# Optimization experiments

Hardware: AMD Instinct MI355X
Metric: run time of the kernel (lower is better)

The kernel has to match this reference:

```python
import jax, jax.numpy as jnp
import numpy as np

EMBED = 1024
HEADS = 16
HEAD_DIM = EMBED // HEADS
LN_EPS = 1e-5
XNORM_GAMMA = 0.01


def xnorm(x, gamma):
    # x * gamma / ||x||_4 along last dim (keepdim)
    norm4 = jnp.sum(x ** 4, axis=-1, keepdims=True) ** 0.25
    return x * gamma / norm4


def setup_inputs() -> dict:
    key = jax.random.key(0)
    ks = jax.random.split(key, 12)
    B, S = 2, 2048
    sc_hd = 1.0 / np.sqrt(HEAD_DIM)
    sc_e = 1.0 / np.sqrt(EMBED)
    return {
        "value": jax.random.normal(ks[0], (B, S, EMBED), jnp.float32),
        "key": jax.random.normal(ks[1], (B, S, EMBED), jnp.float32),
        "query": jax.random.normal(ks[2], (B, S, EMBED), jnp.float32),
        # per-head projections, torch Linear convention: y = x @ W.T
        "Wq": jax.random.normal(ks[3], (HEAD_DIM, HEAD_DIM), jnp.float32) * sc_hd,
        "Wk": jax.random.normal(ks[4], (HEAD_DIM, HEAD_DIM), jnp.float32) * sc_hd,
        "Wv": jax.random.normal(ks[5], (HEAD_DIM, HEAD_DIM), jnp.float32) * sc_hd,
        "Wo": jax.random.normal(ks[6], (EMBED, EMBED), jnp.float32) * sc_e,
        "bo": jnp.zeros((EMBED,), jnp.float32),
        "ln_w": jnp.ones((EMBED,), jnp.float32),
        "ln_b": jnp.zeros((EMBED,), jnp.float32),
        "Wsq": jax.random.normal(ks[7], (EMBED, EMBED), jnp.float32) * sc_e,
        "bsq": jnp.zeros((EMBED,), jnp.float32),
    }


def reference(value, key, query, Wq, Wk, Wv, Wo, bo, ln_w, ln_b, Wsq, bsq):
    B, S, E = query.shape
    # split heads: [B, S, H, D]
    v = value.reshape(B, S, HEADS, HEAD_DIM)
    k = key.reshape(B, S, HEADS, HEAD_DIM)
    q = query.reshape(B, S, HEADS, HEAD_DIM)
    v = jnp.einsum('nshd,ed->nshe', v, Wv)
    k = jnp.einsum('nshd,ed->nshe', k, Wk)
    q = jnp.einsum('nshd,ed->nshe', q, Wq)
    # energy: [B, H, Sq, Sk]
    energy = jnp.einsum('nqhd,nkhd->nhqk', q, k)
    energy_n = xnorm(energy, XNORM_GAMMA)
    v_n = xnorm(v, XNORM_GAMMA)
    out = jnp.einsum('nhql,nlhd->nqhd', energy_n, v_n).reshape(B, S, E)
    attn = out @ Wo.T + bo
    # LayerNorm(attention + query) over embed dim
    x = attn + query
    mu = jnp.mean(x, axis=-1, keepdims=True)
    var = jnp.mean((x - mu) ** 2, axis=-1, keepdims=True)
    x = (x - mu) / jnp.sqrt(var + LN_EPS) * ln_w + ln_b
    # SE gating: x * sigmoid(Linear(x))
    gate = jax.nn.sigmoid(x @ Wsq.T + bsq)
    return x * gate
```

## Files before the change

### kernel.cpp

```cpp
#include <hip/hip_runtime.h>
#include <stdint.h>

#define B_ 2
#define S_ 2048
#define E_ 1024
#define H_ 16
#define HD_ 64
#define N_ (B_*S_)
#define BH_ (B_*H_)
#define GAMMA 0.01f

typedef __attribute__((ext_vector_type(8))) short bf16x8;
typedef __attribute__((ext_vector_type(4))) float f32x4;
typedef __attribute__((ext_vector_type(2))) float f32x2;
typedef __attribute__((ext_vector_type(16))) float f32x16;
typedef unsigned short u16;
typedef unsigned int u32;

#define SWZ(row, kb) ((kb) ^ (((row)&7)<<4))

__device__ __forceinline__ u16 f2bf(float f){
  union { float f; u32 u; } v; v.f = f;
  return (u16)((v.u + 0x7FFFu + ((v.u>>16)&1u)) >> 16);
}

__device__ __forceinline__ float bf2f(u16 u){
  union { u32 u; float f; } v; v.u = ((u32)u)<<16; return v.f;
}

__device__ __forceinline__ u32 cvt_pk_bf16(float lo, float hi){
  u32 r; asm("v_cvt_pk_bf16_f32 %0, %1, %2" : "=v"(r) : "v"(lo), "v"(hi)); return r;
}

__device__ __forceinline__ uint4 pack8(float4 a, float4 b){
  uint4 r;
  r.x = cvt_pk_bf16(a.x, a.y);
  r.y = cvt_pk_bf16(a.z, a.w);
  r.z = cvt_pk_bf16(b.x, b.y);
  r.w = cvt_pk_bf16(b.z, b.w);
  return r;
}

__device__ __forceinline__ bf16x8 ldfrag(const unsigned char* base, int row, int kbyte){
  return *reinterpret_cast<const bf16x8*>(base + row*128 + SWZ(row, kbyte));
}

__device__ __forceinline__ void gl_lds16(const void* g, void* l){
  __builtin_amdgcn_global_load_lds(
      (const __attribute__((address_space(1))) unsigned int*)g,
      (__attribute__((address_space(3))) unsigned int*)l, 16, 0, 0);
}

__device__ __forceinline__ void proj_mfma(const unsigned char* X, const unsigned char* W,
                                          int wid, int l15, int g4, f32x4 acc[4])
{
  f32x4 z = {0.f,0.f,0.f,0.f};
  acc[0]=z; acc[1]=z; acc[2]=z; acc[3]=z;
  #pragma unroll
  for (int kk=0;kk<2;++kk){
    int kbyte = kk*64 + g4*16;
    bf16x8 a = ldfrag(X, wid*16 + l15, kbyte);
    #pragma unroll
    for (int t=0;t<4;++t){
      bf16x8 w = ldfrag(W, t*16 + l15, kbyte);
      acc[t] = __builtin_amdgcn_mfma_f32_16x16x32_bf16(a, w, acc[t], 0, 0, 0);
    }
  }
}

__global__ __launch_bounds__(256) void k_proj(
    const float* __restrict__ qin, const float* __restrict__ kin, const float* __restrict__ vin,
    const float* __restrict__ Wq, const float* __restrict__ Wk, const float* __restrict__ Wv,
    u16* __restrict__ qp, u16* __restrict__ kp, u16* __restrict__ kpT, u16* __restrict__ vnT,
    const float* __restrict__ Wo, const float* __restrict__ Wsq,
    u16* __restrict__ wo16, u16* __restrict__ wsq16)
{
  __shared__ alignas(16) unsigned char sm[49152];
  if (blockIdx.y >= H_){
    int cblk = (blockIdx.y - H_)*64 + blockIdx.x;
    int n4 = (E_*E_)/4;
    for (int i = cblk*256 + threadIdx.x; i < 2*n4; i += 128*256){
      const float4* src; ushort4* dst; int j;
      if (i < n4){ src=(const float4*)Wo;  dst=(ushort4*)wo16;  j=i; }
      else       { src=(const float4*)Wsq; dst=(ushort4*)wsq16; j=i-n4; }
      float4 v = src[j];
      ushort4 p; p.x=f2bf(v.x); p.y=f2bf(v.y); p.z=f2bf(v.z); p.w=f2bf(v.w);
      dst[j] = p;
    }
    return;
  }
  const int XQ=0, XK=8192, XV=16384, WQS=24576, WKS=32768, WVS=40960;
  int tid = threadIdx.x, lane = tid&63, wid = tid>>6;
  int l15 = lane&15, g4 = lane>>4;
  int tb = blockIdx.x*64;
  int h  = blockIdx.y;
  int b  = tb >> 11;
  int sbase = tb & 2047;
  int bh = b*H_ + h;

  {
    int rl = tid>>2;
    int d0 = (tid&3)*16;
    const float* xs[3] = { qin, kin, vin };
    const float* wsrc[3] = { Wq, Wk, Wv };
    const int xoff[3] = {XQ,XK,XV}, woff[3] = {WQS,WKS,WVS};
    #pragma unroll
    for (int m3=0;m3<3;++m3){
      const float4* gx = reinterpret_cast<const float4*>(xs[m3] + (size_t)(tb+rl)*E_ + h*HD_ + d0);
      float4 a=gx[0], bb=gx[1], c=gx[2], d=gx[3];
      *(uint4*)(sm + xoff[m3] + rl*128 + SWZ(rl, d0*2))    = pack8(a,bb);
      *(uint4*)(sm + xoff[m3] + rl*128 + SWZ(rl, d0*2+16)) = pack8(c,d);
      const float4* gw = reinterpret_cast<const float4*>(wsrc[m3] + rl*64 + d0);
      float4 e=gw[0], f=gw[1], g2=gw[2], h2=gw[3];
      *(uint4*)(sm + woff[m3] + rl*128 + SWZ(rl, d0*2))    = pack8(e,f);
      *(uint4*)(sm + woff[m3] + rl*128 + SWZ(rl, d0*2+16)) = pack8(g2,h2);
    }
  }
  __syncthreads();

  f32x4 qacc[4], kacc[4], vacc[4];
  proj_mfma(sm+XQ, sm+WQS, wid, l15, g4, qacc);
  proj_mfma(sm+XK, sm+WKS, wid, l15, g4, kacc);
  proj_mfma(sm+XV, sm+WVS, wid, l15, g4, vacc);

  {
    float p4r[4] = {0.f,0.f,0.f,0.f};
    #pragma unroll
    for (int t=0;t<4;++t)
      #pragma unroll
      for (int r=0;r<4;++r){ float e = vacc[t][r]; float e2 = e*e; p4r[r] += e2*e2; }
    #pragma unroll
    for (int r=0;r<4;++r){
      float p = p4r[r];
      p += __shfl_xor(p,1); p += __shfl_xor(p,2); p += __shfl_xor(p,4); p += __shfl_xor(p,8);
      p4r[r] = GAMMA / sqrtf(sqrtf(p));
    }
    #pragma unroll
    for (int t=0;t<4;++t)
      #pragma unroll
      for (int r=0;r<4;++r) vacc[t][r] *= p4r[r];
  }

  __syncthreads();

  #pragma unroll
  for (int t=0;t<4;++t){
    int dd = t*16 + l15;
    #pragma unroll
    for (int r=0;r<4;++r){
      int tokl = wid*16 + g4*4 + r;
      *(u16*)(sm + XQ + tokl*128 + SWZ(tokl, dd*2)) = f2bf(qacc[t][r]);
      *(u16*)(sm + XK + tokl*128 + SWZ(tokl, dd*2)) = f2bf(kacc[t][r]);
    }
    #pragma unroll
    for (int r=0;r<4;r+=2){
      int tokl = wid*16 + g4*4 + r;
      *(u32*)(sm + XV  + dd*128 + SWZ(dd, tokl*2)) = cvt_pk_bf16(vacc[t][r], vacc[t][r+1]);
      *(u32*)(sm + WQS + dd*128 + SWZ(dd, tokl*2)) = cvt_pk_bf16(kacc[t][r], kacc[t][r+1]);
    }
  }
  __syncthreads();

  {
    int rl = tid>>2; int c2 = tid&3;
    uint4 q0 = *(const uint4*)(sm + XQ + rl*128 + SWZ(rl, c2*32));
    uint4 q1 = *(const uint4*)(sm + XQ + rl*128 + SWZ(rl, c2*32+16));
    size_t qg = ((size_t)bh*S_ + sbase + rl)*HD_ + c2*16;
    *(uint4*)(qp + qg)     = q0;
    *(uint4*)(qp + qg + 8) = q1;
    uint4 k0 = *(const uint4*)(sm + XK + rl*128 + SWZ(rl, c2*32));
    uint4 k1 = *(const uint4*)(sm + XK + rl*128 + SWZ(rl, c2*32+16));
    *(uint4*)(kp + qg)     = k0;
    *(uint4*)(kp + qg + 8) = k1;
    size_t vg = ((size_t)bh*HD_ + rl)*S_ + sbase + c2*16;
    uint4 v0 = *(const uint4*)(sm + XV + rl*128 + SWZ(rl, c2*32));
    uint4 v1 = *(const uint4*)(sm + XV + rl*128 + SWZ(rl, c2*32+16));
    *(uint4*)(vnT + vg)     = v0;
    *(uint4*)(vnT + vg + 8) = v1;
    uint4 t0 = *(const uint4*)(sm + WQS + rl*128 + SWZ(rl, c2*32));
    uint4 t1 = *(const uint4*)(sm + WQS + rl*128 + SWZ(rl, c2*32+16));
    *(uint4*)(kpT + vg)     = t0;
    *(uint4*)(kpT + vg + 8) = t1;
  }
}

__global__ __launch_bounds__(256) void k_kv(
    const u16* __restrict__ kpT, const u16* __restrict__ vnT, u16* __restrict__ MT)
{
  __shared__ alignas(128) unsigned char sm[32768];
  char* smc = (char*)sm;
  int tid = threadIdx.x, lane = tid&63, wv = tid>>6;
  int l31 = lane&31, hi = lane>>5;
  int bh = blockIdx.x;
  const u16* kt = kpT + (size_t)bh*HD_*S_;
  const u16* vt = vnT + (size_t)bh*HD_*S_;

  f32x16 acc[2][2] = {{{}, {}}, {{}, {}}};
  int sbase = wv*512 + hi*8;

  #pragma unroll 2
  for (int it=0; it<32; ++it){
    int so = sbase + it*16;
    bf16x8 ka0 = *reinterpret_cast<const bf16x8*>(kt + (size_t)l31*S_      + so);
    bf16x8 ka1 = *reinterpret_cast<const bf16x8*>(kt + (size_t)(32+l31)*S_ + so);
    bf16x8 vb0 = *reinterpret_cast<const bf16x8*>(vt + (size_t)l31*S_      + so);
    bf16x8 vb1 = *reinterpret_cast<const bf16x8*>(vt + (size_t)(32+l31)*S_ + so);
    acc[0][0] = __builtin_amdgcn_mfma_f32_32x32x16_bf16(ka0, vb0, acc[0][0], 0,0,0);
    acc[0][1] = __builtin_amdgcn_mfma_f32_32x32x16_bf16(ka1, vb0, acc[0][1], 0,0,0);
    acc[1][0] = __builtin_amdgcn_mfma_f32_32x32x16_bf16(ka0, vb1, acc[1][0], 0,0,0);
    acc[1][1] = __builtin_amdgcn_mfma_f32_32x32x16_bf16(ka1, vb1, acc[1][1], 0,0,0);
  }

  auto wrAcc = [&](int sl){
    float* base = (float*)(smc + sl*16384);
    #pragma unroll
    for (int eh=0;eh<2;++eh)
      #pragma unroll
      for (int dh=0;dh<2;++dh){
        float* dst = base + (((eh*2+dh)*64 + lane)*16);
        #pragma unroll
        for (int r4=0;r4<4;++r4)
          *(float4*)(dst + r4*4) = make_float4(acc[eh][dh][r4*4],acc[eh][dh][r4*4+1],
                                               acc[eh][dh][r4*4+2],acc[eh][dh][r4*4+3]);
      }
  };
  auto addAcc = [&](int sl){
    const float* base = (const float*)(smc + sl*16384);
    #pragma unroll
    for (int eh=0;eh<2;++eh)
      #pragma unroll
      for (int dh=0;dh<2;++dh){
        const float* srcp = base + (((eh*2+dh)*64 + lane)*16);
        #pragma unroll
        for (int r4=0;r4<4;++r4){
          float4 t = *(const float4*)(srcp + r4*4);
          acc[eh][dh][r4*4]+=t.x; acc[eh][dh][r4*4+1]+=t.y;
          acc[eh][dh][r4*4+2]+=t.z; acc[eh][dh][r4*4+3]+=t.w;
        }
      }
  };

  if (wv==1) wrAcc(0);
  if (wv==3) wrAcc(1);
  __syncthreads();
  if (wv==0) addAcc(0);
  if (wv==2) addAcc(1);
  __syncthreads();
  if (wv==2) wrAcc(0);
  __syncthreads();
  if (wv==0) addAcc(0);
  __syncthreads();
  if (wv==0){
    #pragma unroll
    for (int eh=0;eh<2;++eh)
      #pragma unroll
      for (int dh=0;dh<2;++dh)
        #pragma unroll
        for (int r=0;r<16;r+=2){
          int e = eh*32 + l31;
          int d = dh*32 + (r&3) + 8*(r>>2) + 4*hi;
          *(u32*)(smc + e*128 + SWZ(e, d*2)) = cvt_pk_bf16(acc[eh][dh][r], acc[eh][dh][r+1]);
        }
  }
  __syncthreads();
  if (wv==0){
    u16* dst = MT + (size_t)bh*4096 + lane*64;
    #pragma unroll
    for (int c=0;c<8;++c)
      *(uint4*)(dst + c*8) = *(const uint4*)(smc + lane*128 + SWZ(lane, c*16));
  }
}

__global__ __launch_bounds__(256, 2) void k_attn(
    const u16* __restrict__ qp, const u16* __restrict__ kp,
    const u16* __restrict__ MT, u16* __restrict__ ao)
{
  __shared__ alignas(128) unsigned char sm[49152];
  __shared__ float px[256];
  char* smc = (char*)sm;
  int tid = threadIdx.x, lane = tid&63, wv = tid>>6;
  int l31 = lane&31, hi = lane>>5;
  int qi = wv>>1, kj = wv&1;
  int L = blockIdx.x;
  int xcd = L&7, iw = L>>3;
  int bh = xcd*4 + (iw>>4);
  int qx = iw&15;
  int qb = qx*128;
  int b = bh>>4, h = bh&15;
  const u16* Kb = kp + (size_t)bh*S_*HD_;
  const u16* Qb = qp + (size_t)bh*S_*HD_;
  int q0 = qb + qi*64;

  bf16x8 qf[2][4];
  #pragma unroll
  for (int f=0;f<2;++f)
    #pragma unroll
    for (int kk=0;kk<4;++kk)
      qf[f][kk] = *reinterpret_cast<const bf16x8*>(Qb + (size_t)(q0 + f*32 + l31)*HD_ + kk*16 + hi*8);

  f32x16 z16 = {};
  f32x2 p4a[2] = {{0.f,0.f},{0.f,0.f}};
  f32x2 p4b[2] = {{0.f,0.f},{0.f,0.f}};

  const char* kSrcC[4];
  #pragma unroll
  for (int c=0;c<4;++c){
    int rk = wv*32 + c*8 + (lane>>3);
    int ck = ((lane&7)*16) ^ ((rk&7)<<4);
    kSrcC[c] = (const char*)Kb + (size_t)rk*128 + ck;
  }

  auto STAGE_K = [&](int bsel, int kt){
    char* db = smc + bsel*16384 + wv*4096;
    #pragma unroll
    for (int c=0;c<4;++c) gl_lds16(kSrcC[c] + (size_t)kt*16384, db + c*1024);
  };

  auto P4ACC = [&](const f32x16& e, f32x2& pa){
    #pragma unroll
    for (int j=0;j<8;++j){
      f32x2 pr = {e[2*j], e[2*j+1]};
      f32x2 e2;
      asm("v_pk_mul_f32 %0, %1, %1" : "=v"(e2) : "v"(pr));
      asm("v_pk_fma_f32 %0, %1, %1, %0" : "+v"(pa) : "v"(e2));
    }
  };

  auto QK = [&](const unsigned char* K_, int s2, f32x16& E0, f32x16& E1){
    bf16x8 ka[4];
    #pragma unroll
    for (int kk=0;kk<4;++kk) ka[kk] = ldfrag(K_, kj*64 + s2*32 + l31, kk*32 + hi*16);
    E0 = z16; E1 = z16;
    __builtin_amdgcn_s_setprio(1);
    #pragma unroll
    for (int kk=0;kk<4;++kk){
      E0 = __builtin_amdgcn_mfma_f32_32x32x16_bf16(ka[kk], qf[0][kk], E0, 0,0,0);
      E1 = __builtin_amdgcn_mfma_f32_32x32x16_bf16(ka[kk], qf[1][kk], E1, 0,0,0);
    }
    __builtin_amdgcn_s_setprio(0);
  };

  const int NT = S_/128;
  STAGE_K(0, 0); STAGE_K(1, 1);

  f32x16 eA0, eA1, eB0, eB1;

  #pragma unroll 1
  for (int t=0; t<NT; ++t){
    if (t < NT-1) { asm volatile("s_waitcnt vmcnt(4)" ::: "memory"); }
    else          { asm volatile("s_waitcnt vmcnt(0)" ::: "memory"); }
    __builtin_amdgcn_s_barrier();
    asm volatile("" ::: "memory");
    if (t+2 < NT) STAGE_K((t+2)%3, t+2);

    const unsigned char* K_ = sm + (t%3)*16384;
    QK(K_, 0, eA0, eA1);
    QK(K_, 1, eB0, eB1);
    P4ACC(eA0, p4a[0]);
    P4ACC(eA1, p4a[1]);
    P4ACC(eB0, p4b[0]);
    P4ACC(eB1, p4b[1]);
  }

  float p4f[2];
  #pragma unroll
  for (int f=0;f<2;++f){
    p4f[f] = p4a[f].x + p4a[f].y + p4b[f].x + p4b[f].y;
    p4f[f] += __shfl_xor(p4f[f], 32);
  }
  __syncthreads();
  if (hi==0){
    px[((qi*2+0)*2+kj)*32 + l31] = p4f[0];
    px[((qi*2+1)*2+kj)*32 + l31] = p4f[1];
  }
  __syncthreads();
  #pragma unroll
  for (int f=0;f<2;++f) p4f[f] += px[((qi*2+f)*2+(1-kj))*32 + l31];
  float sc0 = GAMMA * rsqrtf(sqrtf(p4f[0]));
  float sc1 = GAMMA * rsqrtf(sqrtf(p4f[1]));

  const u16* mtb = MT + (size_t)bh*4096;
  bf16x8 mtf[4];
  #pragma unroll
  for (int kk=0;kk<4;++kk)
    mtf[kk] = *reinterpret_cast<const bf16x8*>(mtb + (kj*32 + l31)*64 + kk*16 + hi*8);
  f32x16 oA0 = z16, oA1 = z16;
  #pragma unroll
  for (int kk=0;kk<4;++kk){
    oA0 = __builtin_amdgcn_mfma_f32_32x32x16_bf16(mtf[kk], qf[0][kk], oA0, 0,0,0);
    oA1 = __builtin_amdgcn_mfma_f32_32x32x16_bf16(mtf[kk], qf[1][kk], oA1, 0,0,0);
  }

  __syncthreads();
  #pragma unroll
  for (int r=0;r<16;r+=2){
    int e = kj*32 + (r&3) + 8*(r>>2) + 4*hi;
    int ql0 = qi*64 + l31;
    *(u32*)(smc + ql0*128 + SWZ(ql0, e*2))         = cvt_pk_bf16(oA0[r]*sc0, oA0[r+1]*sc0);
    int ql1 = qi*64 + 32 + l31;
    *(u32*)(smc + ql1*128 + SWZ(ql1, e*2))         = cvt_pk_bf16(oA1[r]*sc1, oA1[r+1]*sc1);
  }
  __syncthreads();
  {
    int row = tid>>1, eh = tid&1;
    u16* dst = ao + ((size_t)b*S_ + qb + row)*E_ + h*HD_ + eh*32;
    #pragma unroll
    for (int c=0;c<4;++c)
      *(uint4*)(dst + c*8) = *(const uint4*)(smc + row*128 + SWZ(row, eh*64 + c*16));
  }
}

template<int MODE>
__global__ __launch_bounds__(256, 2) void k_gemm(
    const u16* __restrict__ A, const u16* __restrict__ Bw,
    const float* __restrict__ bias, const float* __restrict__ auxf,
    const u16* __restrict__ aux16, float* __restrict__ out32, u16* __restrict__ out16)
{
  __shared__ alignas(128) unsigned char sm[65536];
  char* smc = (char*)sm;
  int tid = threadIdx.x, lane = tid&63, wv = tid>>6;
  int l31 = lane&31, hi = lane>>5;
  int wr = wv>>1, wc = wv&1;
  int LL = (blockIdx.x & 7)*32 + (blockIdx.x >> 3);
  int mt = LL >> 3, nt = LL & 7;
  int m0 = mt*128, n0 = nt*128;

  const char* aS[4]; const char* bS[4];
  #pragma unroll
  for (int c=0;c<4;++c){
    int off = wv*4096 + c*1024 + lane*16;
    int r = off>>7, cl = off&127;
    int cs = cl ^ ((r&7)<<4);
    aS[c] = (const char*)A  + ((size_t)(m0+r)*E_)*2 + cs;
    bS[c] = (const char*)Bw + ((size_t)(n0+r)*E_)*2 + cs;
  }

  auto STAGE = [&](int bsel, int t){
    char* db = smc + bsel*32768 + wv*4096;
    size_t kb2 = (size_t)t*128;
    #pragma unroll
    for (int c=0;c<4;++c) gl_lds16(aS[c] + kb2, db + c*1024);
    #pragma unroll
    for (int c=0;c<4;++c) gl_lds16(bS[c] + kb2, db + 16384 + c*1024);
  };

  f32x16 acc[2][2] = {{{}, {}}, {{}, {}}};

  const int NK = E_/64;
  STAGE(0, 0); STAGE(1, 1);

  #pragma unroll 1
  for (int t=0; t<NK; ++t){
    if (t < NK-1) { asm volatile("s_waitcnt vmcnt(8)" ::: "memory"); }
    else          { asm volatile("s_waitcnt vmcnt(0)" ::: "memory"); }
    __builtin_amdgcn_s_barrier();
    asm volatile("" ::: "memory");

    const unsigned char* Ap_ = sm + (t&1)*32768;
    const unsigned char* Bp_ = Ap_ + 16384;
    #pragma unroll
    for (int kk=0;kk<4;++kk){
      int kbyte = kk*32 + hi*16;
      bf16x8 a0 = ldfrag(Ap_, wr*64 + l31,      kbyte);
      bf16x8 a1 = ldfrag(Ap_, wr*64 + 32 + l31, kbyte);
      bf16x8 b0 = ldfrag(Bp_, wc*64 + l31,      kbyte);
      bf16x8 b1 = ldfrag(Bp_, wc*64 + 32 + l31, kbyte);
      __builtin_amdgcn_s_setprio(1);
      acc[0][0] = __builtin_amdgcn_mfma_f32_32x32x16_bf16(a0, b0, acc[0][0], 0,0,0);
      acc[0][1] = __builtin_amdgcn_mfma_f32_32x32x16_bf16(a0, b1, acc[0][1], 0,0,0);
      acc[1][0] = __builtin_amdgcn_mfma_f32_32x32x16_bf16(a1, b0, acc[1][0], 0,0,0);
      acc[1][1] = __builtin_amdgcn_mfma_f32_32x32x16_bf16(a1, b1, acc[1][1], 0,0,0);
      __builtin_amdgcn_s_setprio(0);
    }

    asm volatile("" ::: "memory");
    __builtin_amdgcn_s_barrier();
    asm volatile("" ::: "memory");
    if (t+2 < NK) STAGE(t&1, t+2);
  }

  #pragma unroll
  for (int cg=0;cg<2;++cg){
    int col = n0 + wc*64 + cg*32 + l31;
    float bi = bias[col];
    #pragma unroll
    for (int rg=0;rg<2;++rg)
      #pragma unroll
      for (int r=0;r<16;++r){
        int mrow = m0 + wr*64 + rg*32 + (r&3) + 8*(r>>2) + 4*hi;
        size_t idx = (size_t)mrow*E_ + col;
        float v = acc[rg][cg][r] + bi;
        if (MODE == 0){
          out16[idx] = f2bf(v + auxf[idx]);
        } else {
          float gg = 1.f/(1.f + __expf(-v));
          out32[idx] = bf2f(aux16[idx]) * gg;
        }
      }
  }
}

__global__ __launch_bounds__(256) void k_ln(
    const u16* __restrict__ xin, const float* __restrict__ lnw, const float* __restrict__ lnb,
    u16* __restrict__ xout)
{
  __shared__ float red[8];
  __shared__ float stats[2];
  int row = blockIdx.x, tid = threadIdx.x;
  ushort4 xr = reinterpret_cast<const ushort4*>(xin + (size_t)row*E_)[tid];
  float x0 = bf2f(xr.x), x1 = bf2f(xr.y), x2 = bf2f(xr.z), x3 = bf2f(xr.w);
  float s  = x0 + x1 + x2 + x3;
  float s2 = x0*x0 + x1*x1 + x2*x2 + x3*x3;
  #pragma unroll
  for (int m=1;m<64;m<<=1){ s += __shfl_xor(s,m); s2 += __shfl_xor(s2,m); }
  if ((tid&63)==0){ red[tid>>6] = s; red[4+(tid>>6)] = s2; }
  __syncthreads();
  if (tid==0){
    float ts  = red[0]+red[1]+red[2]+red[3];
    float ts2 = red[4]+red[5]+red[6]+red[7];
    float mu  = ts * (1.f/E_);
    float var = ts2 * (1.f/E_) - mu*mu;
    stats[0] = mu; stats[1] = rsqrtf(var + 1e-5f);
  }
  __syncthreads();
  float mu = stats[0], rstd = stats[1];
  float4 w  = reinterpret_cast<const float4*>(lnw)[tid];
  float4 bb = reinterpret_cast<const float4*>(lnb)[tid];
  ushort4 p;
  p.x = f2bf((x0-mu)*rstd*w.x + bb.x);
  p.y = f2bf((x1-mu)*rstd*w.y + bb.y);
  p.z = f2bf((x2-mu)*rstd*w.z + bb.z);
  p.w = f2bf((x3-mu)*rstd*w.w + bb.w);
  reinterpret_cast<ushort4*>(xout + (size_t)row*E_)[tid] = p;
}

extern "C" void kernel_launch(void* const* d_in, const int* in_sizes, int n_in,
                              void* d_out, int out_size, void* d_ws, size_t ws_size,
                              hipStream_t stream)
{
  const float* value = (const float*)d_in[0];
  const float* key   = (const float*)d_in[1];
  const float* query = (const float*)d_in[2];
  const float* Wq    = (const float*)d_in[3];
  const float* Wk    = (const float*)d_in[4];
  const float* Wv    = (const float*)d_in[5];
  const float* Wo    = (const float*)d_in[6];
  const float* bo    = (const float*)d_in[7];
  const float* lnw   = (const float*)d_in[8];
  const float* lnb   = (const float*)d_in[9];
  const float* Wsq   = (const float*)d_in[10];
  const float* bsq   = (const float*)d_in[11];
  float* out = (float*)d_out;

  char* ws = (char*)d_ws;
  const size_t MB = 1ull<<20;
  u16*   qp     = (u16*)(ws + 0*MB);
  u16*   kp     = (u16*)(ws + 8*MB);
  u16*   vnT    = (u16*)(ws + 16*MB);
  u16*   kpT    = (u16*)(ws + 24*MB);
  u16*   ao     = (u16*)(ws + 32*MB);
  u16*   mtw    = (u16*)(ws + 44*MB);
  u16*   xres16 = (u16*)(ws + 8*MB);
  u16*   x16    = (u16*)(ws + 16*MB);
  u16*   wo16   = (u16*)(ws + 48*MB);
  u16*   wsq16  = (u16*)(ws + 50*MB);

  k_proj<<<dim3(N_/64, H_+2), 256, 0, stream>>>(query, key, value, Wq, Wk, Wv,
                                                qp, kp, kpT, vnT, Wo, Wsq, wo16, wsq16);
  k_kv  <<<BH_, 256, 0, stream>>>(kpT, vnT, mtw);
  k_attn<<<512, 256, 0, stream>>>(qp, kp, mtw, ao);
  k_gemm<0><<<256, 256, 0, stream>>>(ao, wo16, bo, query, (const u16*)nullptr, (float*)nullptr, xres16);
  k_ln  <<<N_, 256, 0, stream>>>(xres16, lnw, lnb, x16);
  k_gemm<1><<<256, 256, 0, stream>>>(x16, wsq16, bsq, (const float*)nullptr, x16, out, (u16*)nullptr);
}
```

Measured before the change: 111.8 us.

## Split K^T V reduction across more blocks with a separate reduce kernel

```diff
diff --git a/kernel.cpp b/kernel.cpp
--- a/kernel.cpp
+++ b/kernel.cpp
@@ -185,89 +185,82 @@
 }
 
 __global__ __launch_bounds__(256) void k_kv(
-    const u16* __restrict__ kpT, const u16* __restrict__ vnT, u16* __restrict__ MT)
-{
-  __shared__ alignas(128) unsigned char sm[32768];
+    const u16* __restrict__ kpT, const u16* __restrict__ vnT, float* __restrict__ part)
+{
+  __shared__ alignas(128) unsigned char sm[65536];
   char* smc = (char*)sm;
   int tid = threadIdx.x, lane = tid&63, wv = tid>>6;
   int l31 = lane&31, hi = lane>>5;
-  int bh = blockIdx.x;
-  const u16* kt = kpT + (size_t)bh*HD_*S_;
-  const u16* vt = vnT + (size_t)bh*HD_*S_;
+  int bh = blockIdx.x >> 3, ch = blockIdx.x & 7;
+  const char* kt = (const char*)(kpT + (size_t)bh*HD_*S_ + ch*256);
+  const char* vt = (const char*)(vnT + (size_t)bh*HD_*S_ + ch*256);
+
+  #pragma unroll
+  for (int c=0;c<8;++c){
+    int off = wv*8192 + c*1024 + lane*16;
+    int row = off>>9, sl = (off&511)>>4;
+    int ssl = sl ^ (row&31);
+    gl_lds16(kt + (size_t)row*S_*2 + ssl*16, smc + off);
+    gl_lds16(vt + (size_t)row*S_*2 + ssl*16, smc + 32768 + off);
+  }
+  asm volatile("s_waitcnt vmcnt(0)" ::: "memory");
+  __builtin_amdgcn_s_barrier();
+  asm volatile("" ::: "memory");
+
+  auto LD = [&](int mo, int row, int byte) -> bf16x8 {
+    return *reinterpret_cast<const bf16x8*>(smc + mo + row*512 + (byte ^ ((row&31)<<4)));
+  };
 
   f32x16 acc[2][2] = {{{}, {}}, {{}, {}}};
-  int sbase = wv*512 + hi*8;
-
-  #pragma unroll 2
-  for (int it=0; it<32; ++it){
-    int so = sbase + it*16;
-    bf16x8 ka0 = *reinterpret_cast<const bf16x8*>(kt + (size_t)l31*S_      + so);
-    bf16x8 ka1 = *reinterpret_cast<const bf16x8*>(kt + (size_t)(32+l31)*S_ + so);
-    bf16x8 vb0 = *reinterpret_cast<const bf16x8*>(vt + (size_t)l31*S_      + so);
-    bf16x8 vb1 = *reinterpret_cast<const bf16x8*>(vt + (size_t)(32+l31)*S_ + so);
+  #pragma unroll
+  for (int it=0; it<4; ++it){
+    int kb = wv*128 + it*32 + hi*16;
+    bf16x8 ka0 = LD(0,     l31,    kb);
+    bf16x8 ka1 = LD(0,     32+l31, kb);
+    bf16x8 vb0 = LD(32768, l31,    kb);
+    bf16x8 vb1 = LD(32768, 32+l31, kb);
     acc[0][0] = __builtin_amdgcn_mfma_f32_32x32x16_bf16(ka0, vb0, acc[0][0], 0,0,0);
     acc[0][1] = __builtin_amdgcn_mfma_f32_32x32x16_bf16(ka1, vb0, acc[0][1], 0,0,0);
     acc[1][0] = __builtin_amdgcn_mfma_f32_32x32x16_bf16(ka0, vb1, acc[1][0], 0,0,0);
     acc[1][1] = __builtin_amdgcn_mfma_f32_32x32x16_bf16(ka1, vb1, acc[1][1], 0,0,0);
   }
 
-  auto wrAcc = [&](int sl){
-    float* base = (float*)(smc + sl*16384);
-    #pragma unroll
-    for (int eh=0;eh<2;++eh)
+  float* dstw = part + ((size_t)blockIdx.x*4 + wv)*4096;
+  #pragma unroll
+  for (int eh=0;eh<2;++eh)
+    #pragma unroll
+    for (int dh=0;dh<2;++dh){
+      float* d2 = dstw + ((eh*2+dh)*64 + lane)*16;
       #pragma unroll
-      for (int dh=0;dh<2;++dh){
-        float* dst = base + (((eh*2+dh)*64 + lane)*16);
-        #pragma unroll
-        for (int r4=0;r4<4;++r4)
-          *(float4*)(dst + r4*4) = make_float4(acc[eh][dh][r4*4],acc[eh][dh][r4*4+1],
-                                               acc[eh][dh][r4*4+2],acc[eh][dh][r4*4+3]);
-      }
-  };
-  auto addAcc = [&](int sl){
-    const float* base = (const float*)(smc + sl*16384);
-    #pragma unroll
-    for (int eh=0;eh<2;++eh)
-      #pragma unroll
-      for (int dh=0;dh<2;++dh){
-        const float* srcp = base + (((eh*2+dh)*64 + lane)*16);
-        #pragma unroll
-        for (int r4=0;r4<4;++r4){
-          float4 t = *(const float4*)(srcp + r4*4);
-          acc[eh][dh][r4*4]+=t.x; acc[eh][dh][r4*4+1]+=t.y;
-          acc[eh][dh][r4*4+2]+=t.z; acc[eh][dh][r4*4+3]+=t.w;
-        }
-      }
-  };
-
-  if (wv==1) wrAcc(0);
-  if (wv==3) wrAcc(1);
-  __syncthreads();
-  if (wv==0) addAcc(0);
-  if (wv==2) addAcc(1);
-  __syncthreads();
-  if (wv==2) wrAcc(0);
-  __syncthreads();
-  if (wv==0) addAcc(0);
-  __syncthreads();
-  if (wv==0){
-    #pragma unroll
-    for (int eh=0;eh<2;++eh)
-      #pragma unroll
-      for (int dh=0;dh<2;++dh)
-        #pragma unroll
-        for (int r=0;r<16;r+=2){
-          int e = eh*32 + l31;
-          int d = dh*32 + (r&3) + 8*(r>>2) + 4*hi;
-          *(u32*)(smc + e*128 + SWZ(e, d*2)) = cvt_pk_bf16(acc[eh][dh][r], acc[eh][dh][r+1]);
-        }
-  }
-  __syncthreads();
-  if (wv==0){
-    u16* dst = MT + (size_t)bh*4096 + lane*64;
-    #pragma unroll
-    for (int c=0;c<8;++c)
-      *(uint4*)(dst + c*8) = *(const uint4*)(smc + lane*128 + SWZ(lane, c*16));
+      for (int r4=0;r4<4;++r4)
+        *(float4*)(d2 + r4*4) = make_float4(acc[eh][dh][r4*4],acc[eh][dh][r4*4+1],
+                                            acc[eh][dh][r4*4+2],acc[eh][dh][r4*4+3]);
+    }
+}
+
+__global__ __launch_bounds__(256) void k_kvr(
+    const float* __restrict__ part, u16* __restrict__ MT)
+{
+  int tid = threadIdx.x, lane = tid&63, quad = tid>>6;
+  int l31 = lane&31, hi = lane>>5;
+  int bh = blockIdx.x;
+  float s[16] = {0,0,0,0,0,0,0,0,0,0,0,0,0,0,0,0};
+  #pragma unroll 4
+  for (int p=0;p<32;++p){
+    const float* src = part + ((size_t)(bh*8 + (p>>2))*4 + (p&3))*4096 + (quad*64 + lane)*16;
+    #pragma unroll
+    for (int r4=0;r4<4;++r4){
+      float4 t = *(const float4*)(src + r4*4);
+      s[r4*4]+=t.x; s[r4*4+1]+=t.y; s[r4*4+2]+=t.z; s[r4*4+3]+=t.w;
+    }
+  }
+  int eh = quad>>1, dh = quad&1;
+  int e = eh*32 + l31;
+  u16* dst = MT + (size_t)bh*4096 + e*64;
+  #pragma unroll
+  for (int r=0;r<16;r+=2){
+    int d = dh*32 + (r&3) + 8*(r>>2) + 4*hi;
+    *(u32*)(dst + d) = cvt_pk_bf16(s[r], s[r+1]);
   }
 }
 
@@ -396,9 +389,9 @@
   for (int r=0;r<16;r+=2){
     int e = kj*32 + (r&3) + 8*(r>>2) + 4*hi;
     int ql0 = qi*64 + l31;
-    *(u32*)(smc + ql0*128 + SWZ(ql0, e*2))         = cvt_pk_bf16(oA0[r]*sc0, oA0[r+1]*sc0);
+    *(u32*)(smc + ql0*128 + SWZ(ql0, e*2)) = cvt_pk_bf16(oA0[r]*sc0, oA0[r+1]*sc0);
     int ql1 = qi*64 + 32 + l31;
-    *(u32*)(smc + ql1*128 + SWZ(ql1, e*2))         = cvt_pk_bf16(oA1[r]*sc1, oA1[r+1]*sc1);
+    *(u32*)(smc + ql1*128 + SWZ(ql1, e*2)) = cvt_pk_bf16(oA1[r]*sc1, oA1[r+1]*sc1);
   }
   __syncthreads();
   {
@@ -562,12 +555,14 @@
   u16*   mtw    = (u16*)(ws + 44*MB);
   u16*   xres16 = (u16*)(ws + 8*MB);
   u16*   x16    = (u16*)(ws + 16*MB);
+  float* part   = (float*)(ws + 64*MB);
   u16*   wo16   = (u16*)(ws + 48*MB);
   u16*   wsq16  = (u16*)(ws + 50*MB);
 
   k_proj<<<dim3(N_/64, H_+2), 256, 0, stream>>>(query, key, value, Wq, Wk, Wv,
                                                 qp, kp, kpT, vnT, Wo, Wsq, wo16, wsq16);
-  k_kv  <<<BH_, 256, 0, stream>>>(kpT, vnT, mtw);
+  k_kv  <<<256, 256, 0, stream>>>(kpT, vnT, part);
+  k_kvr <<<BH_, 256, 0, stream>>>(part, mtw);
   k_attn<<<512, 256, 0, stream>>>(qp, kp, mtw, ao);
   k_gemm<0><<<256, 256, 0, stream>>>(ao, wo16, bo, query, (const u16*)nullptr, (float*)nullptr, xres16);
   k_ln  <<<N_, 256, 0, stream>>>(xres16, lnw, lnb, x16);
```

New measurement: 111.1 us. Within noise of the previous version (-0.7%).
